# Kernel optimization log

Measured on AMD Instinct MI355X. Metric: run time of the kernel, lower is better.

Reference implementation:

```python
import jax, jax.numpy as jnp
import numpy as np

N = 8192          # num_nodes
E = 262144        # num_edges = N * avg_degree(32)
K_SIGN = 1000.0   # ExactModel k
EPSILON = 5.0     # ExactModel epsilon


def setup_inputs() -> dict:
    key = jax.random.key(0)
    k1, k2, k3, k4 = jax.random.split(key, 4)
    src = jax.random.randint(k1, (E,), 0, N)
    dst = jax.random.randint(k2, (E,), 0, N)
    edge_index = jnp.stack([src, dst]).astype(jnp.int32)          # (2, E)
    # partition vector, elements in {1, ..., N}
    p = jax.random.randint(k3, (N,), 1, N + 1).astype(jnp.float32)  # (N,)
    x = jax.random.normal(k4, (N, 1), dtype=jnp.float32)            # node features
    return {"edge_index": edge_index, "p": p, "x": x}


def reference(edge_index, p, x):
    """infoco1 (segment logsumexp over edges with self-loops) followed by one
    refine step: pairwise difference matrix + CustomSignFunction tanh + row-sum."""
    n = p.shape[0]
    log_n = jnp.log(jnp.asarray(n, dtype=p.dtype))
    loops = jnp.arange(n, dtype=edge_index.dtype)
    src = jnp.concatenate([edge_index[0], loops])   # add_self_loops
    dst = jnp.concatenate([edge_index[1], loops])
    # contributions_log = log(p_i) + p_j * log(N)
    contrib = jnp.log(p[src]) + p[dst] * log_n      # (E + N,)
    # numerically stable segment log-sum-exp over incoming edges of each node
    mx = jax.ops.segment_max(contrib, dst, num_segments=n)              # scatter_max
    se = jax.ops.segment_sum(jnp.exp(contrib - mx[dst]), dst, num_segments=n)  # scatter_add
    S = mx + jnp.log(se) + jnp.dot(x[:, 0], p)      # infoco1: S_log + <x, p>
    # refine: all-pairs sign refinement, D_1 = tanh(k * (X - X^T) - eps)
    X = S[:, None]                                   # (N, 1)
    D1 = jnp.tanh(K_SIGN * (X - X.T) - EPSILON)      # (N, N)
    return D1.sum(axis=1)                            # (N,)
```

## Files before the change

### kernel.cpp

```cpp
#include <hip/hip_runtime.h>
#include <math.h>

#define K_SIGN 1000.0f
#define EPSILON 5.0f

#define D_HI ((EPSILON + 12.0f) / K_SIGN)
#define D_LO ((EPSILON - 12.0f) / K_SIGN)

#define NB_HIST 64


__global__ void __launch_bounds__(256) k_hist(
        const int* __restrict__ src, const int* __restrict__ dst,
        const float* __restrict__ p, const float* __restrict__ x,
        int* __restrict__ Hpriv, double* __restrict__ C,
        int* __restrict__ PFX, int* __restrict__ order, int e, int n) {
    __shared__ int buf[8192];
    __shared__ int pl[8192];
    __shared__ int csum[256];
    __shared__ double dred[4];
    int tid = threadIdx.x;
    int b = blockIdx.x;

    int4* b4 = (int4*)buf;
    const float4* p4 = (const float4*)p;
    int4* pl4 = (int4*)pl;
    for (int i = tid; i < n / 4; i += 256) {
        b4[i] = make_int4(0, 0, 0, 0);
        float4 v = p4[i];
        pl4[i] = make_int4((int)v.x, (int)v.y, (int)v.z, (int)v.w);
    }
    __syncthreads();

    if (b < NB_HIST) {
        int per = e / NB_HIST;
        int base = b * per;
        int4 s4[4], d4[4];
#pragma unroll
        for (int k = 0; k < 4; ++k) {
            int off = base + (k * 256 + tid) * 4;
            s4[k] = *(const int4*)(src + off);
            d4[k] = *(const int4*)(dst + off);
        }
#pragma unroll
        for (int k = 0; k < 4; ++k) {
            atomicAdd(&buf[d4[k].x], pl[s4[k].x]);
            atomicAdd(&buf[d4[k].y], pl[s4[k].y]);
            atomicAdd(&buf[d4[k].z], pl[s4[k].z]);
            atomicAdd(&buf[d4[k].w], pl[s4[k].w]);
        }
        __syncthreads();
        int4* o4 = (int4*)(Hpriv + b * n);
        for (int i = tid; i < n / 4; i += 256) o4[i] = b4[i];
        return;
    }

    double acc = 0.0;
    for (int i = tid; i < n; i += 256) {
        float pv = p[i];
        atomicAdd(&buf[(int)pv - 1], 1);
        acc += (double)x[i] * (double)pv;
    }
    for (int off = 32; off > 0; off >>= 1)
        acc += __shfl_down(acc, off, 64);
    if ((tid & 63) == 0) dred[tid >> 6] = acc;
    __syncthreads();
    if (tid == 0) *C = dred[0] + dred[1] + dred[2] + dred[3];

    int cw = n / 256;
    int base = tid * cw;
    int s = 0;
    for (int k = 0; k < cw; ++k) s += buf[base + k];
    csum[tid] = s;
    __syncthreads();
    for (int off = 1; off < 256; off <<= 1) {
        int v = (tid >= off) ? csum[tid - off] : 0;
        __syncthreads();
        csum[tid] += v;
        __syncthreads();
    }
    int run = (tid == 0) ? 0 : csum[tid - 1];
    for (int k = 0; k < cw; ++k) {
        int h = buf[base + k];
        PFX[base + k] = run;
        buf[base + k] = run;
        run += h;
    }
    if (tid == 0) PFX[n] = n;
    __syncthreads();

    for (int i = tid; i < n; i += 256) {
        int r = atomicAdd(&buf[(int)p[i] - 1], 1);
        order[r] = i;
    }
}

__global__ void __launch_bounds__(256) k_merge(
        const int* __restrict__ Hpriv, const float* __restrict__ p,
        const double* __restrict__ C, float* __restrict__ S,
        int n, float log_n) {
    __shared__ int part[8][32];
    int lane = threadIdx.x & 31;
    int slice = threadIdx.x >> 5;
    int i = blockIdx.x * 32 + lane;
    int s = 0;
#pragma unroll
    for (int h = slice * 8; h < slice * 8 + 8; ++h)
        s += Hpriv[h * n + i];
    part[slice][lane] = s;
    __syncthreads();
    if (threadIdx.x < 32) {
        int t = 0;
#pragma unroll
        for (int q = 0; q < 8; ++q) t += part[q][lane];
        float pv = p[i];
        t += (int)pv;
        S[i] = (logf((float)t) + pv * log_n) + (float)(*C);
    }
}

__global__ void __launch_bounds__(64) k_out(const float* __restrict__ S,
                                            const float* __restrict__ p,
                                            const int* __restrict__ PFX,
                                            const int* __restrict__ order,
                                            float* __restrict__ out, int n) {
    int i = blockIdx.x * 64 + threadIdx.x;
    if (i >= n) return;
    int pi = (int)p[i];
    int base = PFX[pi - 1];
    int g = PFX[pi] - base;
    float si = S[i];
    float acc = (float)(base - (n - base - g));
    for (int k = 0; k < g; ++k) {
        int j = order[base + k];
        float d = si - S[j];
        if (d > D_HI) acc += 1.0f;
        else if (d < D_LO) acc -= 1.0f;
        else acc += tanhf(fmaf(K_SIGN, d, -EPSILON));
    }
    out[i] = acc;
}

extern "C" void kernel_launch(void* const* d_in, const int* in_sizes, int n_in,
                              void* d_out, int out_size, void* d_ws, size_t ws_size,
                              hipStream_t stream) {
    const int* edge_index = (const int*)d_in[0];
    const float* p = (const float*)d_in[1];
    const float* x = (const float*)d_in[2];
    float* out = (float*)d_out;

    int e = in_sizes[0] / 2;
    int n = in_sizes[1];
    const int* src = edge_index;
    const int* dst = edge_index + e;

    double* C = (double*)d_ws;
    float* S = (float*)((char*)d_ws + 16);
    int* PFX = (int*)(S + n);
    int* order = PFX + (n + 4);
    int* Hpriv = order + n;

    float log_n = logf((float)n);

    k_hist<<<NB_HIST + 1, 256, 0, stream>>>(src, dst, p, x, Hpriv, C,
                                            PFX, order, e, n);
    k_merge<<<n / 32, 256, 0, stream>>>(Hpriv, p, C, S, n, log_n);
    k_out<<<n / 64, 64, 0, stream>>>(S, p, PFX, order, out, n);
}
```

Baseline: 96.82 us.

## Fuse histogram, merge and output kernels into one cooperative kernel with grid syncs

Replaces the three separate launches (histogram, merge, output) with one cooperative kernel. Its phases are separated by `__threadfence` plus `cg::this_grid().sync()`, launched through `hipLaunchCooperativeKernel` with 65 blocks. It also stops building an integer copy of `p` in shared memory and instead gathers `p[src]` from global memory straight into registers before the shared atomics. The aim is to remove per-launch overhead and the shared-table setup cost. In exchange, the merge and output phases now run on only 65 blocks instead of hundreds, and each thread serially sums 64 histogram rows, so there is less parallelism and added grid-barrier cost.

Result: slower. 143.8 us (+48.5%).

```diff
diff --git a/kernel.cpp b/kernel.cpp
--- a/kernel.cpp
+++ b/kernel.cpp
@@ -1,5 +1,8 @@
 #include <hip/hip_runtime.h>
+#include <hip/hip_cooperative_groups.h>
 #include <math.h>
+
+namespace cg = cooperative_groups;
 
 #define K_SIGN 1000.0f
 #define EPSILON 5.0f
@@ -8,33 +11,28 @@
 #define D_LO ((EPSILON - 12.0f) / K_SIGN)
 
 #define NB_HIST 64
+#define NBLK (NB_HIST + 1)
 
 
-__global__ void __launch_bounds__(256) k_hist(
+__global__ void __launch_bounds__(256) k_all(
         const int* __restrict__ src, const int* __restrict__ dst,
         const float* __restrict__ p, const float* __restrict__ x,
         int* __restrict__ Hpriv, double* __restrict__ C,
-        int* __restrict__ PFX, int* __restrict__ order, int e, int n) {
+        int* __restrict__ PFX, int* __restrict__ order,
+        float* __restrict__ S, float* __restrict__ out,
+        int e, int n, float log_n) {
     __shared__ int buf[8192];
-    __shared__ int pl[8192];
     __shared__ int csum[256];
     __shared__ double dred[4];
     int tid = threadIdx.x;
     int b = blockIdx.x;
 
     int4* b4 = (int4*)buf;
-    const float4* p4 = (const float4*)p;
-    int4* pl4 = (int4*)pl;
-    for (int i = tid; i < n / 4; i += 256) {
-        b4[i] = make_int4(0, 0, 0, 0);
-        float4 v = p4[i];
-        pl4[i] = make_int4((int)v.x, (int)v.y, (int)v.z, (int)v.w);
-    }
+    for (int i = tid; i < n / 4; i += 256) b4[i] = make_int4(0, 0, 0, 0);
     __syncthreads();
 
     if (b < NB_HIST) {
-        int per = e / NB_HIST;
-        int base = b * per;
+        int base = b * (e / NB_HIST);
         int4 s4[4], d4[4];
 #pragma unroll
         for (int k = 0; k < 4; ++k) {
@@ -42,103 +40,96 @@
             s4[k] = *(const int4*)(src + off);
             d4[k] = *(const int4*)(dst + off);
         }
+        int pv[16];
 #pragma unroll
         for (int k = 0; k < 4; ++k) {
-            atomicAdd(&buf[d4[k].x], pl[s4[k].x]);
-            atomicAdd(&buf[d4[k].y], pl[s4[k].y]);
-            atomicAdd(&buf[d4[k].z], pl[s4[k].z]);
-            atomicAdd(&buf[d4[k].w], pl[s4[k].w]);
+            pv[4 * k + 0] = (int)p[s4[k].x];
+            pv[4 * k + 1] = (int)p[s4[k].y];
+            pv[4 * k + 2] = (int)p[s4[k].z];
+            pv[4 * k + 3] = (int)p[s4[k].w];
+        }
+#pragma unroll
+        for (int k = 0; k < 4; ++k) {
+            atomicAdd(&buf[d4[k].x], pv[4 * k + 0]);
+            atomicAdd(&buf[d4[k].y], pv[4 * k + 1]);
+            atomicAdd(&buf[d4[k].z], pv[4 * k + 2]);
+            atomicAdd(&buf[d4[k].w], pv[4 * k + 3]);
         }
         __syncthreads();
         int4* o4 = (int4*)(Hpriv + b * n);
         for (int i = tid; i < n / 4; i += 256) o4[i] = b4[i];
-        return;
+    } else {
+        double acc = 0.0;
+        for (int i = tid; i < n; i += 256) {
+            float pv = p[i];
+            atomicAdd(&buf[(int)pv - 1], 1);
+            acc += (double)x[i] * (double)pv;
+        }
+        for (int off = 32; off > 0; off >>= 1)
+            acc += __shfl_down(acc, off, 64);
+        if ((tid & 63) == 0) dred[tid >> 6] = acc;
+        __syncthreads();
+        if (tid == 0) *C = dred[0] + dred[1] + dred[2] + dred[3];
+
+        int cw = n / 256;
+        int base = tid * cw;
+        int s = 0;
+        for (int k = 0; k < cw; ++k) s += buf[base + k];
+        csum[tid] = s;
+        __syncthreads();
+        for (int off = 1; off < 256; off <<= 1) {
+            int v = (tid >= off) ? csum[tid - off] : 0;
+            __syncthreads();
+            csum[tid] += v;
+            __syncthreads();
+        }
+        int run = (tid == 0) ? 0 : csum[tid - 1];
+        for (int k = 0; k < cw; ++k) {
+            int h = buf[base + k];
+            PFX[base + k] = run;
+            buf[base + k] = run;
+            run += h;
+        }
+        if (tid == 0) PFX[n] = n;
+        __syncthreads();
+
+        for (int i = tid; i < n; i += 256) {
+            int r = atomicAdd(&buf[(int)p[i] - 1], 1);
+            order[r] = i;
+        }
     }
 
-    double acc = 0.0;
-    for (int i = tid; i < n; i += 256) {
-        float pv = p[i];
-        atomicAdd(&buf[(int)pv - 1], 1);
-        acc += (double)x[i] * (double)pv;
+    __threadfence();
+    cg::this_grid().sync();
+
+    int gid = b * 256 + tid;
+    if (gid < n) {
+        int t = 0;
+#pragma unroll 8
+        for (int h = 0; h < NB_HIST; ++h) t += Hpriv[h * n + gid];
+        float pv = p[gid];
+        t += (int)pv;
+        S[gid] = (logf((float)t) + pv * log_n) + (float)(*C);
     }
-    for (int off = 32; off > 0; off >>= 1)
-        acc += __shfl_down(acc, off, 64);
-    if ((tid & 63) == 0) dred[tid >> 6] = acc;
-    __syncthreads();
-    if (tid == 0) *C = dred[0] + dred[1] + dred[2] + dred[3];
 
-    int cw = n / 256;
-    int base = tid * cw;
-    int s = 0;
-    for (int k = 0; k < cw; ++k) s += buf[base + k];
-    csum[tid] = s;
-    __syncthreads();
-    for (int off = 1; off < 256; off <<= 1) {
-        int v = (tid >= off) ? csum[tid - off] : 0;
-        __syncthreads();
-        csum[tid] += v;
-        __syncthreads();
+    __threadfence();
+    cg::this_grid().sync();
+
+    if (gid < n) {
+        int pi = (int)p[gid];
+        int base = PFX[pi - 1];
+        int g = PFX[pi] - base;
+        float si = S[gid];
+        float acc = (float)(base - (n - base - g));
+        for (int k = 0; k < g; ++k) {
+            int j = order[base + k];
+            float d = si - S[j];
+            if (d > D_HI) acc += 1.0f;
+            else if (d < D_LO) acc -= 1.0f;
+            else acc += tanhf(fmaf(K_SIGN, d, -EPSILON));
+        }
+        out[gid] = acc;
     }
-    int run = (tid == 0) ? 0 : csum[tid - 1];
-    for (int k = 0; k < cw; ++k) {
-        int h = buf[base + k];
-        PFX[base + k] = run;
-        buf[base + k] = run;
-        run += h;
-    }
-    if (tid == 0) PFX[n] = n;
-    __syncthreads();
-
-    for (int i = tid; i < n; i += 256) {
-        int r = atomicAdd(&buf[(int)p[i] - 1], 1);
-        order[r] = i;
-    }
-}
-
-__global__ void __launch_bounds__(256) k_merge(
-        const int* __restrict__ Hpriv, const float* __restrict__ p,
-        const double* __restrict__ C, float* __restrict__ S,
-        int n, float log_n) {
-    __shared__ int part[8][32];
-    int lane = threadIdx.x & 31;
-    int slice = threadIdx.x >> 5;
-    int i = blockIdx.x * 32 + lane;
-    int s = 0;
-#pragma unroll
-    for (int h = slice * 8; h < slice * 8 + 8; ++h)
-        s += Hpriv[h * n + i];
-    part[slice][lane] = s;
-    __syncthreads();
-    if (threadIdx.x < 32) {
-        int t = 0;
-#pragma unroll
-        for (int q = 0; q < 8; ++q) t += part[q][lane];
-        float pv = p[i];
-        t += (int)pv;
-        S[i] = (logf((float)t) + pv * log_n) + (float)(*C);
-    }
-}
-
-__global__ void __launch_bounds__(64) k_out(const float* __restrict__ S,
-                                            const float* __restrict__ p,
-                                            const int* __restrict__ PFX,
-                                            const int* __restrict__ order,
-                                            float* __restrict__ out, int n) {
-    int i = blockIdx.x * 64 + threadIdx.x;
-    if (i >= n) return;
-    int pi = (int)p[i];
-    int base = PFX[pi - 1];
-    int g = PFX[pi] - base;
-    float si = S[i];
-    float acc = (float)(base - (n - base - g));
-    for (int k = 0; k < g; ++k) {
-        int j = order[base + k];
-        float d = si - S[j];
-        if (d > D_HI) acc += 1.0f;
-        else if (d < D_LO) acc -= 1.0f;
-        else acc += tanhf(fmaf(K_SIGN, d, -EPSILON));
-    }
-    out[i] = acc;
 }
 
 extern "C" void kernel_launch(void* const* d_in, const int* in_sizes, int n_in,
@@ -162,8 +153,10 @@
 
     float log_n = logf((float)n);
 
-    k_hist<<<NB_HIST + 1, 256, 0, stream>>>(src, dst, p, x, Hpriv, C,
-                                            PFX, order, e, n);
-    k_merge<<<n / 32, 256, 0, stream>>>(Hpriv, p, C, S, n, log_n);
-    k_out<<<n / 64, 64, 0, stream>>>(S, p, PFX, order, out, n);
+    void* args[] = {(void*)&src, (void*)&dst, (void*)&p, (void*)&x,
+                    (void*)&Hpriv, (void*)&C, (void*)&PFX, (void*)&order,
+                    (void*)&S, (void*)&out, (void*)&e, (void*)&n,
+                    (void*)&log_n};
+    hipLaunchCooperativeKernel((const void*)k_all, dim3(NBLK), dim3(256),
+                               args, 0, stream);
 }
```
